# Performance work log

Hardware: AMD Instinct MI355X
Metric: run time of the kernel (lower is better)

The kernel has to match this reference:

```python
import jax, jax.numpy as jnp
import numpy as np

B, N, D, H, DK = 4, 2048, 1024, 16, 64  # batch, seq, model_dim, heads, key_dim (= value_dim)
NEG = -1e9


def setup_inputs() -> dict:
    key = jax.random.key(0)
    ks = jax.random.split(key, 5)
    X = jax.random.normal(ks[0], (B, N, D), dtype=jnp.float32)
    # causal additive mask [N, N]; module slices mask[:N, :M] and adds to logits
    mask = jnp.where(jnp.tril(jnp.ones((N, N), dtype=bool)), 0.0, NEG).astype(jnp.float32)
    s = 1.0 / np.sqrt(D)
    Wq = jax.random.normal(ks[1], (D, H * DK), dtype=jnp.float32) * s
    Wk = jax.random.normal(ks[2], (D, H * DK), dtype=jnp.float32) * s
    Wv = jax.random.normal(ks[3], (D, H * DK), dtype=jnp.float32) * s
    Wo = jax.random.normal(ks[4], (H * DK, D), dtype=jnp.float32) * s
    return {"X": X, "mask": mask, "Wq": Wq, "Wk": Wk, "Wv": Wv, "Wo": Wo}


def reference(X, mask, Wq, Wk, Wv, Wo):
    # Linear projections (bias=False), then split heads: [B,N,H,DK] -> [B,H,N,DK]
    Q = (X @ Wq).reshape(B, N, H, DK).transpose(0, 2, 1, 3)
    K = (X @ Wk).reshape(B, N, H, DK).transpose(0, 2, 1, 3)
    V = (X @ Wv).reshape(B, N, H, DK).transpose(0, 2, 1, 3)
    # full [B,H,N,N] attention logits (module materializes it explicitly)
    att = jnp.einsum('bhnd,bhmd->bhnm', Q, K) / jnp.sqrt(jnp.float32(DK))
    # dropout is in eval mode here -> identity; then additive mask[:N,:M]
    att = att + mask[:N, :N]
    prob = jax.nn.softmax(att, axis=-1)
    values = jnp.einsum('bhnm,bhmd->bhnd', prob, V)
    values_cat = values.transpose(0, 2, 1, 3).reshape(B, N, H * DK)
    return values_cat @ Wo
```

## Files before the change

### kernel.cpp

```cpp
#include <hip/hip_runtime.h>

typedef __fp16   f2  __attribute__((ext_vector_type(2)));
typedef _Float16 h4  __attribute__((ext_vector_type(4)));
typedef _Float16 v8h __attribute__((ext_vector_type(8)));
typedef float    v4f __attribute__((ext_vector_type(4)));
struct f2x2 { f2 lo, hi; };

#if __has_builtin(__builtin_amdgcn_exp2f)
#define FEXP2(x) __builtin_amdgcn_exp2f(x)
#else
#define FEXP2(x) exp2f(x)
#endif

constexpr int Bn = 4, Nn = 2048, Dn = 1024, Hn = 16, DKn = 64, Mn = 8192;

__device__ __forceinline__ void load_lds16(const _Float16* g, _Float16* l) {
    __builtin_amdgcn_global_load_lds(
        (const __attribute__((address_space(1))) void*)g,
        (__attribute__((address_space(3))) void*)l, 16, 0, 0);
}

__global__ __launch_bounds__(256) void cast_f16(const float* __restrict__ x,
                                                _Float16* __restrict__ y) {
    const int i = blockIdx.x * 256 + threadIdx.x;
    const float4 v = ((const float4*)x)[i];
    h4 o; o[0] = (_Float16)v.x; o[1] = (_Float16)v.y;
    o[2] = (_Float16)v.z; o[3] = (_Float16)v.w;
    ((h4*)y)[i] = o;
}

__global__ __launch_bounds__(256) void castW4(const float* __restrict__ Wq,
                                              const float* __restrict__ Wk,
                                              const float* __restrict__ Wv,
                                              const float* __restrict__ Wo,
                                              _Float16* __restrict__ Wqkv,
                                              _Float16* __restrict__ Wto) {
    __shared__ float tile[32][33];
    const int which = blockIdx.x >> 10, bid = blockIdx.x & 1023;
    const float* W = which == 0 ? Wq : which == 1 ? Wk : which == 2 ? Wv : Wo;
    _Float16* Dst = which < 3 ? (Wqkv + ((size_t)which << 20)) : Wto;
    const int bx = bid & 31, by = bid >> 5;
    const int t = threadIdx.x;
    const int r = t >> 3, c4 = (t & 7) * 4;
    const float4 v = *(const float4*)&W[(size_t)(by * 32 + r) * Dn + bx * 32 + c4];
    tile[r][c4 + 0] = v.x; tile[r][c4 + 1] = v.y;
    tile[r][c4 + 2] = v.z; tile[r][c4 + 3] = v.w;
    __syncthreads();
    h4 o;
    o[0] = (_Float16)tile[c4 + 0][r];
    o[1] = (_Float16)tile[c4 + 1][r];
    o[2] = (_Float16)tile[c4 + 2][r];
    o[3] = (_Float16)tile[c4 + 3][r];
    *(h4*)&Dst[(size_t)(bx * 32 + r) * Dn + by * 32 + c4] = o;
}

#define MFMA16(A, B, C) __builtin_amdgcn_mfma_f32_16x16x32_f16((A), (B), (C), 0, 0, 0)

#define GEMM_PIPE_SETUP(MF_, NF_, BN_, WME, WNE, VMS)                            \
    constexpr int MF = MF_, NF = NF_, BNc = BN_;                                 \
    constexpr int BREG = BNc * 32;                     \
    __shared__ __align__(16) _Float16 As[4 * 8192];                              \
    __shared__ __align__(16) _Float16 Bs[4 * BREG];                              \
    const int t = threadIdx.x, lane = t & 63, w = t >> 6;                        \
    const int quad = lane >> 4, l16 = lane & 15;                                 \
    const int wm = (WME), wn = (WNE);                                            \
                        \
    const int rA = t >> 2;                                                       \
    const int gc = ((t & 3) ^ ((t >> 3) & 3)) * 8;  \
    const _Float16* pA0 = Abase + (size_t)rA * Dn + gc;                          \
    const _Float16* pA1 = pA0 + (size_t)128 * Dn;           \
    const _Float16* pB0 = Bbase + (size_t)rA * Dn + gc;                          \
    const _Float16* pB1 = pB0 + (size_t)128 * Dn;   \
    auto stage = [&](int ts, int sh) {                                           \
        const int reg = (ts & 1) * 2 + sh;                                       \
        const int ko  = ts * 64 + sh * 32;                                       \
        load_lds16(pA0 + ko, As + reg * 8192 + w * 512);                         \
        load_lds16(pA1 + ko, As + reg * 8192 + 4096 + w * 512);                  \
        load_lds16(pB0 + ko, Bs + reg * BREG + w * 512);                         \
        if (BNc == 256) load_lds16(pB1 + ko, Bs + reg * BREG + 4096 + w * 512);  \
    };                                                                           \
             \
    const int swz  = (quad ^ ((l16 >> 1) & 3)) * 8;                              \
    const int aoff = (wm * (MF * 16) + l16) * 32 + swz;                          \
    const int boff = (wn * (NF * 16) + l16) * 32 + swz;                          \
    v4f acc[MF][NF];                                                             \
    _Pragma("unroll") for (int i = 0; i < MF; ++i)                               \
        _Pragma("unroll") for (int j = 0; j < NF; ++j) acc[i][j] = v4f{0, 0, 0, 0};\
    stage(0, 0); stage(0, 1); stage(1, 0);            \
    asm volatile("s_waitcnt " VMS ::: "memory");                                 \
    __builtin_amdgcn_s_barrier();

#define GPHASE(BUF, KH, TS, SH, DOST, VM) do {                                   \
    const _Float16* Ab_ = As + ((BUF) * 2 + (KH)) * 8192 + aoff;                 \
    const _Float16* Bb_ = Bs + ((BUF) * 2 + (KH)) * BREG + boff;                 \
    v8h a_[MF], b_[NF];                                                          \
    _Pragma("unroll") for (int i = 0; i < MF; ++i)                               \
        a_[i] = *(const v8h*)(Ab_ + i * 512);                                    \
    _Pragma("unroll") for (int j = 0; j < NF; ++j)                               \
        b_[j] = *(const v8h*)(Bb_ + j * 512);                                    \
    if (DOST) stage((TS), (SH));                                                 \
    __builtin_amdgcn_s_barrier();                                                \
    __builtin_amdgcn_s_setprio(1);                                               \
    _Pragma("unroll") for (int i = 0; i < MF; ++i)                               \
        _Pragma("unroll") for (int j = 0; j < NF; ++j)                           \
            acc[i][j] = MFMA16(a_[i], b_[j], acc[i][j]);                         \
    __builtin_amdgcn_s_setprio(0);                                               \
    asm volatile("s_waitcnt " VM ::: "memory");                                  \
    __builtin_amdgcn_s_barrier();                                                \
} while (0)

#define GEMM_PIPE_KLOOP(VMS, VMT)                                                \
    for (int tt = 0; tt < 14; tt += 2) {                                         \
        GPHASE(0, 0, tt + 1, 1, true, VMS);                                      \
        GPHASE(0, 1, tt + 2, 0, true, VMS);                                      \
        GPHASE(1, 0, tt + 2, 1, true, VMS);                                      \
        GPHASE(1, 1, tt + 3, 0, true, VMS);                                      \
    }                                                                            \
    GPHASE(0, 0, 15, 1, true,  VMS);              \
    GPHASE(0, 1, 0, 0, false, VMT);                                    \
    GPHASE(1, 0, 0, 0, false, "vmcnt(0)");                             \
    GPHASE(1, 1, 0, 0, false, "vmcnt(0)");

__global__ __launch_bounds__(512) void gemmqkv(const _Float16* __restrict__ A,
                                               const _Float16* __restrict__ Wt,
                                               _Float16* __restrict__ Qo,
                                               _Float16* __restrict__ Ko,
                                               _Float16* __restrict__ Vo)
{
    const int bx = blockIdx.x % 12, by = blockIdx.x / 12;
    const int m0 = by * 256, n0 = bx * 256;
    const _Float16* Abase = A + (size_t)m0 * Dn;
    const _Float16* Bbase = Wt + (size_t)n0 * Dn;

    GEMM_PIPE_SETUP(8, 4, 256, w >> 2, w & 3, "vmcnt(8)")
    GEMM_PIPE_KLOOP("vmcnt(8)", "vmcnt(4)")

    const int sec = n0 >> 10;
    if (sec < 2) {
        _Float16* C = sec ? Ko : Qo;
        const float scale = sec ? 1.0f : 0.125f * 1.44269504f;
#pragma unroll
        for (int mf = 0; mf < MF; ++mf) {
            const int mbase = m0 + wm * 128 + mf * 16 + quad * 4;
#pragma unroll
            for (int nf = 0; nf < NF; ++nf) {
                const int nl = (n0 + wn * 64 + nf * 16 + l16) & 1023;
                const int h = nl >> 6, dk = nl & 63;
#pragma unroll
                for (int r = 0; r < 4; ++r) {
                    const int m = mbase + r, b = m >> 11, nr = m & (Nn - 1);
                    C[((size_t)(b * Hn + h) * Nn + nr) * DKn + dk] = (_Float16)(acc[mf][nf][r] * scale);
                }
            }
        }
    } else {
#pragma unroll
        for (int mf = 0; mf < MF; ++mf) {
            const int mbase = m0 + wm * 128 + mf * 16 + quad * 4;
            const int b = mbase >> 11, nr = mbase & (Nn - 1);
#pragma unroll
            for (int nf = 0; nf < NF; ++nf) {
                const int nl = (n0 + wn * 64 + nf * 16 + l16) & 1023;
                const int h = nl >> 6, dk = nl & 63;
                h4 o; o[0] = (_Float16)acc[mf][nf][0]; o[1] = (_Float16)acc[mf][nf][1];
                o[2] = (_Float16)acc[mf][nf][2]; o[3] = (_Float16)acc[mf][nf][3];
                *(h4*)&Vo[((size_t)(b * Hn + h) * DKn + dk) * Nn + nr] = o;
            }
        }
    }
}

__global__ __launch_bounds__(512) void gemmo(const _Float16* __restrict__ A,
                                             const _Float16* __restrict__ Wt,
                                             float* __restrict__ C)
{
    const int bx = blockIdx.x & 7, by = blockIdx.x >> 3;
    const int m0 = by * 256, n0 = bx * 128;
    const _Float16* Abase = A + (size_t)m0 * Dn;
    const _Float16* Bbase = Wt + (size_t)n0 * Dn;

    GEMM_PIPE_SETUP(4, 4, 128, w & 3, w >> 2, "vmcnt(6)")
    GEMM_PIPE_KLOOP("vmcnt(6)", "vmcnt(3)")

#pragma unroll
    for (int mf = 0; mf < MF; ++mf) {
        const int mbase = m0 + wm * 64 + mf * 16 + quad * 4;
#pragma unroll
        for (int nf = 0; nf < NF; ++nf) {
            const int n = n0 + wn * 64 + nf * 16 + l16;
#pragma unroll
            for (int r = 0; r < 4; ++r)
                C[(size_t)(mbase + r) * Dn + n] = acc[mf][nf][r];
        }
    }
}

__global__ __launch_bounds__(256) void flashv5(const _Float16* __restrict__ Q,
                                               const _Float16* __restrict__ K,
                                               const _Float16* __restrict__ Vt,
                                               _Float16* __restrict__ O)
{
    __shared__ __align__(16) _Float16 KS[64 * 64];
    __shared__ __align__(16) _Float16 VS[64 * 64];
    __shared__ __align__(16) _Float16 Ps[4][32 * 64];

    const int t = threadIdx.x;
    const int lane = t & 63, w = t >> 6;
    const int quad = lane >> 4, l16 = lane & 15;
    const int bh = blockIdx.x & 63;
    const int qtile = 15 - (blockIdx.x >> 6);
    const int b = bh >> 4, h = bh & 15;
    const int qb = qtile * 128 + w * 32;

    const _Float16* Qg = Q  + (size_t)bh * Nn * DKn;
    const _Float16* Kg = K  + (size_t)bh * Nn * DKn;
    const _Float16* Vg = Vt + (size_t)bh * DKn * Nn;

    auto stage = [&](int kt) {
        const int k0 = kt * 64;
#pragma unroll
        for (int jj = 0; jj < 2; ++jj) {
            const int ci = jj * 256 + w * 64 + lane;
            const int r = ci >> 3, c = ci & 7;
            const int gc = (c ^ (r & 7)) * 8;
            load_lds16(Kg + (size_t)(k0 + r) * DKn + gc, &KS[(jj * 256 + w * 64) * 8]);
            load_lds16(Vg + (size_t)r * Nn + k0 + gc,    &VS[(jj * 256 + w * 64) * 8]);
        }
    };
#define SWZ(arr, r, c) (*(const v8h*)&(arr)[(r) * 64 + (((c) ^ ((r) & 7)) * 8)])

    v8h qf[2][2];
#pragma unroll
    for (int qq = 0; qq < 2; ++qq)
#pragma unroll
        for (int ks = 0; ks < 2; ++ks)
            qf[qq][ks] = *(const v8h*)&Qg[(size_t)(qb + qq * 16 + l16) * DKn + ks * 32 + quad * 8];

    v8h ones;
#pragma unroll
    for (int i = 0; i < 8; ++i) ones[i] = (_Float16)1.0f;

    v4f o[2][4];
#pragma unroll
    for (int mq = 0; mq < 2; ++mq)
#pragma unroll
        for (int nt = 0; nt < 4; ++nt) o[mq][nt] = v4f{0.f, 0.f, 0.f, 0.f};
    v4f ol[2] = {v4f{0.f, 0.f, 0.f, 0.f}, v4f{0.f, 0.f, 0.f, 0.f}};

    const int NKT  = 2 * qtile + 2;
    const int diag = 2 * qtile + (w >> 1);

    for (int kt = 0; kt < NKT; ++kt) {
        stage(kt);
        __syncthreads();
        if (kt <= diag) {
            const int k0 = kt * 64;
            auto ptile = [&](bool domask) {
#pragma unroll
                for (int kk = 0; kk < 4; ++kk) {
                    v4f s0 = v4f{0.f, 0.f, 0.f, 0.f}, s1 = v4f{0.f, 0.f, 0.f, 0.f};
#pragma unroll
                    for (int ks = 0; ks < 2; ++ks) {
                        const v8h ak = SWZ(KS, kk * 16 + l16, ks * 4 + quad);
                        s0 = __builtin_amdgcn_mfma_f32_16x16x32_f16(ak, qf[0][ks], s0, 0, 0, 0);
                        s1 = __builtin_amdgcn_mfma_f32_16x16x32_f16(ak, qf[1][ks], s1, 0, 0, 0);
                    }
                    const int key0 = k0 + kk * 16 + quad * 4;
#pragma unroll
                    for (int qq = 0; qq < 2; ++qq) {
                        const v4f sv = qq ? s1 : s0;
                        const int q = qb + qq * 16 + l16;
                        float p[4];
#pragma unroll
                        for (int r = 0; r < 4; ++r) {
                            float x = sv[r];
                            if (domask) x = (key0 + r > q) ? -1e9f : x;
                            p[r] = FEXP2(x);
                        }
                        f2x2 pkr;
                        pkr.lo = __builtin_amdgcn_cvt_pkrtz(p[0], p[1]);
                        pkr.hi = __builtin_amdgcn_cvt_pkrtz(p[2], p[3]);
                        const h4 pk = __builtin_bit_cast(h4, pkr);
                        const int prow = qq * 16 + l16;
                        const int pch  = kk * 2 + (quad >> 1);
                        *(h4*)&Ps[w][prow * 64 + ((pch ^ (prow & 7)) * 8 + (quad & 1) * 4)] = pk;
                    }
                }
#pragma unroll
                for (int ks = 0; ks < 2; ++ks)
#pragma unroll
                    for (int mq = 0; mq < 2; ++mq) {
                        const int arow = mq * 16 + l16;
                        const int ach  = ks * 4 + quad;
                        const v8h a = *(const v8h*)&Ps[w][arow * 64 + ((ach ^ (arow & 7)) * 8)];
#pragma unroll
                        for (int nt = 0; nt < 4; ++nt) {
                            const v8h bvv = SWZ(VS, nt * 16 + l16, ks * 4 + quad);
                            o[mq][nt] = __builtin_amdgcn_mfma_f32_16x16x32_f16(a, bvv, o[mq][nt], 0, 0, 0);
                        }
                        ol[mq] = __builtin_amdgcn_mfma_f32_16x16x32_f16(a, ones, ol[mq], 0, 0, 0);
                    }
            };
            if (kt == diag) ptile(true); else ptile(false);
        }
        __syncthreads();
    }
#undef SWZ

    _Float16* Op = O + (size_t)b * Nn * Dn + h * DKn;
#pragma unroll
    for (int mq = 0; mq < 2; ++mq)
#pragma unroll
        for (int r = 0; r < 4; ++r) {
            const float li = 1.0f / ol[mq][r];
            const int qrow = qb + mq * 16 + quad * 4 + r;
#pragma unroll
            for (int nt = 0; nt < 4; ++nt)
                Op[(size_t)qrow * Dn + nt * 16 + l16] = (_Float16)(o[mq][nt][r] * li);
        }
}

extern "C" void kernel_launch(void* const* d_in, const int* in_sizes, int n_in,
                              void* d_out, int out_size, void* d_ws, size_t ws_size,
                              hipStream_t stream)
{
    const float* X  = (const float*)d_in[0];
    const float* Wq = (const float*)d_in[2];
    const float* Wk = (const float*)d_in[3];
    const float* Wv = (const float*)d_in[4];
    const float* Wo = (const float*)d_in[5];

    char* ws = (char*)d_ws;
    _Float16* Xh   = (_Float16*)ws;
    _Float16* Wqkv = (_Float16*)(ws + (16u << 20));
    _Float16* Wto  = Wqkv + (3u << 20);
    _Float16* Qh   = Wto + (1u << 20);
    _Float16* Kh   = Qh + (size_t)Mn * Dn;
    _Float16* Vth  = Kh + (size_t)Mn * Dn;
    _Float16* Ah   = Vth + (size_t)Mn * Dn;

    cast_f16<<<(Mn * Dn / 4) / 256, 256, 0, stream>>>(X, Xh);
    castW4<<<4096, 256, 0, stream>>>(Wq, Wk, Wv, Wo, Wqkv, Wto);
    gemmqkv<<<384, 512, 0, stream>>>(Xh, Wqkv, Qh, Kh, Vth);
    flashv5<<<1024, 256, 0, stream>>>(Qh, Kh, Vth, Ah);
    gemmo<<<256, 512, 0, stream>>>(Ah, Wto, (float*)d_out);
}
```

Before: 262.1 us.

## Double-buffer GEMM LDS fragment reads in registers to overlap with MFMA

The GEMM k-loop now loads the next LDS fragment set into a second register bank while the MFMAs run on the previous set, and drops the mid-phase barrier between the LDS read and the compute. The vmcnt waits are tightened because each phase now reads one region ahead, so global loads must land earlier. This aims to hide LDS read latency behind matrix math, at the cost of more VGPRs for the doubled fragment registers and less slack for global-load latency.

```diff
diff --git a/kernel.cpp b/kernel.cpp
--- a/kernel.cpp
+++ b/kernel.cpp
@@ -86,40 +86,47 @@
     v4f acc[MF][NF];                                                             \
     _Pragma("unroll") for (int i = 0; i < MF; ++i)                               \
         _Pragma("unroll") for (int j = 0; j < NF; ++j) acc[i][j] = v4f{0, 0, 0, 0};\
+    v8h aR0[MF], aR1[MF], bR0[NF], bR1[NF];                                      \
     stage(0, 0); stage(0, 1); stage(1, 0);            \
-    asm volatile("s_waitcnt " VMS ::: "memory");                                 \
-    __builtin_amdgcn_s_barrier();
-
-#define GPHASE(BUF, KH, TS, SH, DOST, VM) do {                                   \
-    const _Float16* Ab_ = As + ((BUF) * 2 + (KH)) * 8192 + aoff;                 \
-    const _Float16* Bb_ = Bs + ((BUF) * 2 + (KH)) * BREG + boff;                 \
-    v8h a_[MF], b_[NF];                                                          \
+    asm volatile("s_waitcnt " VMS ::: "memory");         \
+    __builtin_amdgcn_s_barrier();                                                \
+    GRD(0, 0);
+
+#define GRD(SET, REG) do {                                                       \
+    const _Float16* Ab_ = As + (REG) * 8192 + aoff;                              \
+    const _Float16* Bb_ = Bs + (REG) * BREG + boff;                              \
     _Pragma("unroll") for (int i = 0; i < MF; ++i)                               \
-        a_[i] = *(const v8h*)(Ab_ + i * 512);                                    \
+        aR##SET[i] = *(const v8h*)(Ab_ + i * 512);                               \
     _Pragma("unroll") for (int j = 0; j < NF; ++j)                               \
-        b_[j] = *(const v8h*)(Bb_ + j * 512);                                    \
-    if (DOST) stage((TS), (SH));                                                 \
-    __builtin_amdgcn_s_barrier();                                                \
+        bR##SET[j] = *(const v8h*)(Bb_ + j * 512);                               \
+} while (0)
+
+#define GMM(SET)                                                                 \
     __builtin_amdgcn_s_setprio(1);                                               \
     _Pragma("unroll") for (int i = 0; i < MF; ++i)                               \
         _Pragma("unroll") for (int j = 0; j < NF; ++j)                           \
-            acc[i][j] = MFMA16(a_[i], b_[j], acc[i][j]);                         \
-    __builtin_amdgcn_s_setprio(0);                                               \
+            acc[i][j] = MFMA16(aR##SET[i], bR##SET[j], acc[i][j]);               \
+    __builtin_amdgcn_s_setprio(0);
+
+#define GPHASE(RSET, RREG, MSET, TS, SH, DOST, VM) do {                          \
+    GRD(RSET, RREG);                                                             \
+    if (DOST) stage((TS), (SH));                                                 \
+    GMM(MSET)                                                                    \
     asm volatile("s_waitcnt " VM ::: "memory");                                  \
     __builtin_amdgcn_s_barrier();                                                \
 } while (0)
 
-#define GEMM_PIPE_KLOOP(VMS, VMT)                                                \
+#define GEMM_PIPE_KLOOP(VMS)                                                     \
     for (int tt = 0; tt < 14; tt += 2) {                                         \
-        GPHASE(0, 0, tt + 1, 1, true, VMS);                                      \
-        GPHASE(0, 1, tt + 2, 0, true, VMS);                                      \
-        GPHASE(1, 0, tt + 2, 1, true, VMS);                                      \
-        GPHASE(1, 1, tt + 3, 0, true, VMS);                                      \
+        GPHASE(1, 1, 0, tt + 1, 1, true, VMS);                                   \
+        GPHASE(0, 2, 1, tt + 2, 0, true, VMS);                                   \
+        GPHASE(1, 3, 0, tt + 2, 1, true, VMS);                                   \
+        GPHASE(0, 0, 1, tt + 3, 0, true, VMS);                                   \
     }                                                                            \
-    GPHASE(0, 0, 15, 1, true,  VMS);              \
-    GPHASE(0, 1, 0, 0, false, VMT);                                    \
-    GPHASE(1, 0, 0, 0, false, "vmcnt(0)");                             \
-    GPHASE(1, 1, 0, 0, false, "vmcnt(0)");
+    GPHASE(1, 1, 0, 15, 1, true,  VMS);           \
+    GPHASE(0, 2, 1, 0, 0, false, "vmcnt(0)");                          \
+    GPHASE(1, 3, 0, 0, 0, false, "vmcnt(0)");                          \
+    GMM(1)
 
 __global__ __launch_bounds__(512) void gemmqkv(const _Float16* __restrict__ A,
                                                const _Float16* __restrict__ Wt,
@@ -132,8 +139,8 @@
     const _Float16* Abase = A + (size_t)m0 * Dn;
     const _Float16* Bbase = Wt + (size_t)n0 * Dn;
 
-    GEMM_PIPE_SETUP(8, 4, 256, w >> 2, w & 3, "vmcnt(8)")
-    GEMM_PIPE_KLOOP("vmcnt(8)", "vmcnt(4)")
+    GEMM_PIPE_SETUP(8, 4, 256, w >> 2, w & 3, "vmcnt(4)")
+    GEMM_PIPE_KLOOP("vmcnt(4)")
 
     const int sec = n0 >> 10;
     if (sec < 2) {
@@ -179,8 +186,8 @@
     const _Float16* Abase = A + (size_t)m0 * Dn;
     const _Float16* Bbase = Wt + (size_t)n0 * Dn;
 
-    GEMM_PIPE_SETUP(4, 4, 128, w & 3, w >> 2, "vmcnt(6)")
-    GEMM_PIPE_KLOOP("vmcnt(6)", "vmcnt(3)")
+    GEMM_PIPE_SETUP(4, 4, 128, w & 3, w >> 2, "vmcnt(3)")
+    GEMM_PIPE_KLOOP("vmcnt(3)")
 
 #pragma unroll
     for (int mf = 0; mf < MF; ++mf) {
```

Result: slower. 275.5 us (+5.1%).

## Split QKV GEMM k-step into two half-phases to cut register pressure

Applied to the files above, without the earlier changes.

Replaces the shared GEMM macros with per-kernel code. The QKV GEMM now loads the A fragments in two halves of four, with a barrier between the MFMA groups, and splits the global-to-LDS staging of A and B across the two halves. Both GEMMs get launch_bounds(512, 2) and explicit lgkmcnt waits. The goal is fewer live VGPRs so two blocks can share a CU, and better interleaving of loads with MFMA work. The cost is extra barriers per k-step and tighter register budgets that may cause spills.

```diff
diff --git a/kernel.cpp b/kernel.cpp
--- a/kernel.cpp
+++ b/kernel.cpp
@@ -56,94 +56,104 @@
 
 #define MFMA16(A, B, C) __builtin_amdgcn_mfma_f32_16x16x32_f16((A), (B), (C), 0, 0, 0)
 
-#define GEMM_PIPE_SETUP(MF_, NF_, BN_, WME, WNE, VMS)                            \
-    constexpr int MF = MF_, NF = NF_, BNc = BN_;                                 \
-    constexpr int BREG = BNc * 32;                     \
-    __shared__ __align__(16) _Float16 As[4 * 8192];                              \
-    __shared__ __align__(16) _Float16 Bs[4 * BREG];                              \
-    const int t = threadIdx.x, lane = t & 63, w = t >> 6;                        \
-    const int quad = lane >> 4, l16 = lane & 15;                                 \
-    const int wm = (WME), wn = (WNE);                                            \
-                        \
-    const int rA = t >> 2;                                                       \
-    const int gc = ((t & 3) ^ ((t >> 3) & 3)) * 8;  \
-    const _Float16* pA0 = Abase + (size_t)rA * Dn + gc;                          \
-    const _Float16* pA1 = pA0 + (size_t)128 * Dn;           \
-    const _Float16* pB0 = Bbase + (size_t)rA * Dn + gc;                          \
-    const _Float16* pB1 = pB0 + (size_t)128 * Dn;   \
-    auto stage = [&](int ts, int sh) {                                           \
-        const int reg = (ts & 1) * 2 + sh;                                       \
-        const int ko  = ts * 64 + sh * 32;                                       \
-        load_lds16(pA0 + ko, As + reg * 8192 + w * 512);                         \
-        load_lds16(pA1 + ko, As + reg * 8192 + 4096 + w * 512);                  \
-        load_lds16(pB0 + ko, Bs + reg * BREG + w * 512);                         \
-        if (BNc == 256) load_lds16(pB1 + ko, Bs + reg * BREG + 4096 + w * 512);  \
-    };                                                                           \
-             \
-    const int swz  = (quad ^ ((l16 >> 1) & 3)) * 8;                              \
-    const int aoff = (wm * (MF * 16) + l16) * 32 + swz;                          \
-    const int boff = (wn * (NF * 16) + l16) * 32 + swz;                          \
-    v4f acc[MF][NF];                                                             \
-    _Pragma("unroll") for (int i = 0; i < MF; ++i)                               \
-        _Pragma("unroll") for (int j = 0; j < NF; ++j) acc[i][j] = v4f{0, 0, 0, 0};\
-    stage(0, 0); stage(0, 1); stage(1, 0);            \
-    asm volatile("s_waitcnt " VMS ::: "memory");                                 \
-    __builtin_amdgcn_s_barrier();
-
-#define GPHASE(BUF, KH, TS, SH, DOST, VM) do {                                   \
-    const _Float16* Ab_ = As + ((BUF) * 2 + (KH)) * 8192 + aoff;                 \
-    const _Float16* Bb_ = Bs + ((BUF) * 2 + (KH)) * BREG + boff;                 \
-    v8h a_[MF], b_[NF];                                                          \
-    _Pragma("unroll") for (int i = 0; i < MF; ++i)                               \
-        a_[i] = *(const v8h*)(Ab_ + i * 512);                                    \
-    _Pragma("unroll") for (int j = 0; j < NF; ++j)                               \
-        b_[j] = *(const v8h*)(Bb_ + j * 512);                                    \
-    if (DOST) stage((TS), (SH));                                                 \
-    __builtin_amdgcn_s_barrier();                                                \
-    __builtin_amdgcn_s_setprio(1);                                               \
-    _Pragma("unroll") for (int i = 0; i < MF; ++i)                               \
-        _Pragma("unroll") for (int j = 0; j < NF; ++j)                           \
-            acc[i][j] = MFMA16(a_[i], b_[j], acc[i][j]);                         \
-    __builtin_amdgcn_s_setprio(0);                                               \
-    asm volatile("s_waitcnt " VM ::: "memory");                                  \
-    __builtin_amdgcn_s_barrier();                                                \
-} while (0)
-
-#define GEMM_PIPE_KLOOP(VMS, VMT)                                                \
-    for (int tt = 0; tt < 14; tt += 2) {                                         \
-        GPHASE(0, 0, tt + 1, 1, true, VMS);                                      \
-        GPHASE(0, 1, tt + 2, 0, true, VMS);                                      \
-        GPHASE(1, 0, tt + 2, 1, true, VMS);                                      \
-        GPHASE(1, 1, tt + 3, 0, true, VMS);                                      \
-    }                                                                            \
-    GPHASE(0, 0, 15, 1, true,  VMS);              \
-    GPHASE(0, 1, 0, 0, false, VMT);                                    \
-    GPHASE(1, 0, 0, 0, false, "vmcnt(0)");                             \
-    GPHASE(1, 1, 0, 0, false, "vmcnt(0)");
-
-__global__ __launch_bounds__(512) void gemmqkv(const _Float16* __restrict__ A,
-                                               const _Float16* __restrict__ Wt,
-                                               _Float16* __restrict__ Qo,
-                                               _Float16* __restrict__ Ko,
-                                               _Float16* __restrict__ Vo)
+__global__ __launch_bounds__(512, 2) void gemmqkv(const _Float16* __restrict__ A,
+                                                  const _Float16* __restrict__ Wt,
+                                                  _Float16* __restrict__ Qo,
+                                                  _Float16* __restrict__ Ko,
+                                                  _Float16* __restrict__ Vo)
 {
+    __shared__ __align__(16) _Float16 As[4 * 8192];
+    __shared__ __align__(16) _Float16 Bs[4 * 8192];
     const int bx = blockIdx.x % 12, by = blockIdx.x / 12;
     const int m0 = by * 256, n0 = bx * 256;
     const _Float16* Abase = A + (size_t)m0 * Dn;
     const _Float16* Bbase = Wt + (size_t)n0 * Dn;
 
-    GEMM_PIPE_SETUP(8, 4, 256, w >> 2, w & 3, "vmcnt(8)")
-    GEMM_PIPE_KLOOP("vmcnt(8)", "vmcnt(4)")
+    const int t = threadIdx.x, lane = t & 63, w = t >> 6;
+    const int quad = lane >> 4, l16 = lane & 15;
+    const int wm = w >> 2, wn = w & 3;
+    const int rA = t >> 2;
+    const int gc = ((t & 3) ^ ((t >> 3) & 3)) * 8;
+    const _Float16* pA0 = Abase + (size_t)rA * Dn + gc;
+    const _Float16* pA1 = pA0 + (size_t)128 * Dn;
+    const _Float16* pB0 = Bbase + (size_t)rA * Dn + gc;
+    const _Float16* pB1 = pB0 + (size_t)128 * Dn;
+    auto stageA = [&](int ts, int sh) {
+        const int reg = (ts & 1) * 2 + sh, ko = ts * 64 + sh * 32;
+        load_lds16(pA0 + ko, As + reg * 8192 + w * 512);
+        load_lds16(pA1 + ko, As + reg * 8192 + 4096 + w * 512);
+    };
+    auto stageB = [&](int ts, int sh) {
+        const int reg = (ts & 1) * 2 + sh, ko = ts * 64 + sh * 32;
+        load_lds16(pB0 + ko, Bs + reg * 8192 + w * 512);
+        load_lds16(pB1 + ko, Bs + reg * 8192 + 4096 + w * 512);
+    };
+    const int swz  = (quad ^ ((l16 >> 1) & 3)) * 8;
+    const int aoff = (wm * 128 + l16) * 32 + swz;
+    const int boff = (wn * 64 + l16) * 32 + swz;
+
+    v4f acc[8][4];
+#pragma unroll
+    for (int i = 0; i < 8; ++i)
+#pragma unroll
+        for (int j = 0; j < 4; ++j) acc[i][j] = v4f{0.f, 0.f, 0.f, 0.f};
+
+    stageA(0, 0); stageB(0, 0); stageA(0, 1); stageB(0, 1); stageA(1, 0); stageB(1, 0);
+    asm volatile("s_waitcnt vmcnt(8)" ::: "memory");
+    __builtin_amdgcn_s_barrier();
+
+#define QKV_KSTEP(REG, TS, SH, DOST, VM, DOVM) do {                              \
+    const _Float16* Ab_ = As + (REG) * 8192 + aoff;                              \
+    const _Float16* Bb_ = Bs + (REG) * 8192 + boff;                              \
+    v8h aL[4], aH[4], bL[4];                                                     \
+    _Pragma("unroll") for (int q2 = 0; q2 < 4; ++q2) {                           \
+        aL[q2] = *(const v8h*)(Ab_ + q2 * 512);                                  \
+        bL[q2] = *(const v8h*)(Bb_ + q2 * 512);                                  \
+    }                                                                            \
+    if (DOST) stageA((TS), (SH));                                                \
+    __builtin_amdgcn_s_barrier();                                                \
+    asm volatile("s_waitcnt lgkmcnt(0)" ::: "memory");                           \
+    __builtin_amdgcn_s_setprio(1);                                               \
+    _Pragma("unroll") for (int i2 = 0; i2 < 4; ++i2)                             \
+        _Pragma("unroll") for (int j2 = 0; j2 < 4; ++j2)                         \
+            acc[i2][j2] = MFMA16(aL[i2], bL[j2], acc[i2][j2]);                   \
+    __builtin_amdgcn_s_setprio(0);                                               \
+    __builtin_amdgcn_s_barrier();                                                \
+    _Pragma("unroll") for (int q2 = 0; q2 < 4; ++q2)                             \
+        aH[q2] = *(const v8h*)(Ab_ + 2048 + q2 * 512);                           \
+    if (DOST) stageB((TS), (SH));                                                \
+    __builtin_amdgcn_s_barrier();                                                \
+    asm volatile("s_waitcnt lgkmcnt(0)" ::: "memory");                           \
+    __builtin_amdgcn_s_setprio(1);                                               \
+    _Pragma("unroll") for (int i2 = 0; i2 < 4; ++i2)                             \
+        _Pragma("unroll") for (int j2 = 0; j2 < 4; ++j2)                         \
+            acc[4 + i2][j2] = MFMA16(aH[i2], bL[j2], acc[4 + i2][j2]);           \
+    __builtin_amdgcn_s_setprio(0);                                               \
+    if (DOVM) asm volatile("s_waitcnt " VM ::: "memory");                        \
+    __builtin_amdgcn_s_barrier();                                                \
+} while (0)
+
+    for (int tt = 0; tt < 14; tt += 2) {
+        QKV_KSTEP(0, tt + 1, 1, true, "vmcnt(8)", true);
+        QKV_KSTEP(1, tt + 2, 0, true, "vmcnt(8)", true);
+        QKV_KSTEP(2, tt + 2, 1, true, "vmcnt(8)", true);
+        QKV_KSTEP(3, tt + 3, 0, true, "vmcnt(8)", true);
+    }
+    QKV_KSTEP(0, 15, 1, true,  "vmcnt(8)", true);
+    QKV_KSTEP(1, 0, 0, false, "vmcnt(4)", true);
+    QKV_KSTEP(2, 0, 0, false, "vmcnt(0)", true);
+    QKV_KSTEP(3, 0, 0, false, "vmcnt(0)", false);
+#undef QKV_KSTEP
 
     const int sec = n0 >> 10;
     if (sec < 2) {
         _Float16* C = sec ? Ko : Qo;
         const float scale = sec ? 1.0f : 0.125f * 1.44269504f;
 #pragma unroll
-        for (int mf = 0; mf < MF; ++mf) {
+        for (int mf = 0; mf < 8; ++mf) {
             const int mbase = m0 + wm * 128 + mf * 16 + quad * 4;
 #pragma unroll
-            for (int nf = 0; nf < NF; ++nf) {
+            for (int nf = 0; nf < 4; ++nf) {
                 const int nl = (n0 + wn * 64 + nf * 16 + l16) & 1023;
                 const int h = nl >> 6, dk = nl & 63;
 #pragma unroll
@@ -155,11 +165,11 @@
         }
     } else {
 #pragma unroll
-        for (int mf = 0; mf < MF; ++mf) {
+        for (int mf = 0; mf < 8; ++mf) {
             const int mbase = m0 + wm * 128 + mf * 16 + quad * 4;
             const int b = mbase >> 11, nr = mbase & (Nn - 1);
 #pragma unroll
-            for (int nf = 0; nf < NF; ++nf) {
+            for (int nf = 0; nf < 4; ++nf) {
                 const int nl = (n0 + wn * 64 + nf * 16 + l16) & 1023;
                 const int h = nl >> 6, dk = nl & 63;
                 h4 o; o[0] = (_Float16)acc[mf][nf][0]; o[1] = (_Float16)acc[mf][nf][1];
@@ -170,23 +180,82 @@
     }
 }
 
-__global__ __launch_bounds__(512) void gemmo(const _Float16* __restrict__ A,
-                                             const _Float16* __restrict__ Wt,
-                                             float* __restrict__ C)
+__global__ __launch_bounds__(512, 2) void gemmo(const _Float16* __restrict__ A,
+                                                const _Float16* __restrict__ Wt,
+                                                float* __restrict__ C)
 {
+    __shared__ __align__(16) _Float16 As[4 * 8192];
+    __shared__ __align__(16) _Float16 Bs[4 * 4096];
     const int bx = blockIdx.x & 7, by = blockIdx.x >> 3;
     const int m0 = by * 256, n0 = bx * 128;
     const _Float16* Abase = A + (size_t)m0 * Dn;
     const _Float16* Bbase = Wt + (size_t)n0 * Dn;
 
-    GEMM_PIPE_SETUP(4, 4, 128, w & 3, w >> 2, "vmcnt(6)")
-    GEMM_PIPE_KLOOP("vmcnt(6)", "vmcnt(3)")
-
-#pragma unroll
-    for (int mf = 0; mf < MF; ++mf) {
+    const int t = threadIdx.x, lane = t & 63, w = t >> 6;
+    const int quad = lane >> 4, l16 = lane & 15;
+    const int wm = w & 3, wn = w >> 2;
+    const int rA = t >> 2;
+    const int gc = ((t & 3) ^ ((t >> 3) & 3)) * 8;
+    const _Float16* pA0 = Abase + (size_t)rA * Dn + gc;
+    const _Float16* pA1 = pA0 + (size_t)128 * Dn;
+    const _Float16* pB0 = Bbase + (size_t)rA * Dn + gc;
+    auto stage3 = [&](int ts, int sh) {
+        const int reg = (ts & 1) * 2 + sh, ko = ts * 64 + sh * 32;
+        load_lds16(pA0 + ko, As + reg * 8192 + w * 512);
+        load_lds16(pA1 + ko, As + reg * 8192 + 4096 + w * 512);
+        load_lds16(pB0 + ko, Bs + reg * 4096 + w * 512);
+    };
+    const int swz  = (quad ^ ((l16 >> 1) & 3)) * 8;
+    const int aoff = (wm * 64 + l16) * 32 + swz;
+    const int boff = (wn * 64 + l16) * 32 + swz;
+
+    v4f acc[4][4];
+#pragma unroll
+    for (int i = 0; i < 4; ++i)
+#pragma unroll
+        for (int j = 0; j < 4; ++j) acc[i][j] = v4f{0.f, 0.f, 0.f, 0.f};
+
+    stage3(0, 0); stage3(0, 1); stage3(1, 0);
+    asm volatile("s_waitcnt vmcnt(6)" ::: "memory");
+    __builtin_amdgcn_s_barrier();
+
+#define O_KSTEP(REG, TS, SH, DOST, VM, DOVM) do {                                \
+    const _Float16* Ab_ = As + (REG) * 8192 + aoff;                              \
+    const _Float16* Bb_ = Bs + (REG) * 4096 + boff;                              \
+    v8h aL[4], bL[4];                                                            \
+    _Pragma("unroll") for (int q2 = 0; q2 < 4; ++q2) {                           \
+        aL[q2] = *(const v8h*)(Ab_ + q2 * 512);                                  \
+        bL[q2] = *(const v8h*)(Bb_ + q2 * 512);                                  \
+    }                                                                            \
+    if (DOST) stage3((TS), (SH));                                                \
+    __builtin_amdgcn_s_barrier();                                                \
+    asm volatile("s_waitcnt lgkmcnt(0)" ::: "memory");                           \
+    __builtin_amdgcn_s_setprio(1);                                               \
+    _Pragma("unroll") for (int i2 = 0; i2 < 4; ++i2)                             \
+        _Pragma("unroll") for (int j2 = 0; j2 < 4; ++j2)                         \
+            acc[i2][j2] = MFMA16(aL[i2], bL[j2], acc[i2][j2]);                   \
+    __builtin_amdgcn_s_setprio(0);                                               \
+    if (DOVM) asm volatile("s_waitcnt " VM ::: "memory");                        \
+    __builtin_amdgcn_s_barrier();                                                \
+} while (0)
+
+    for (int tt = 0; tt < 14; tt += 2) {
+        O_KSTEP(0, tt + 1, 1, true, "vmcnt(6)", true);
+        O_KSTEP(1, tt + 2, 0, true, "vmcnt(6)", true);
+        O_KSTEP(2, tt + 2, 1, true, "vmcnt(6)", true);
+        O_KSTEP(3, tt + 3, 0, true, "vmcnt(6)", true);
+    }
+    O_KSTEP(0, 15, 1, true,  "vmcnt(6)", true);
+    O_KSTEP(1, 0, 0, false, "vmcnt(3)", true);
+    O_KSTEP(2, 0, 0, false, "vmcnt(0)", true);
+    O_KSTEP(3, 0, 0, false, "vmcnt(0)", false);
+#undef O_KSTEP
+
+#pragma unroll
+    for (int mf = 0; mf < 4; ++mf) {
         const int mbase = m0 + wm * 64 + mf * 16 + quad * 4;
 #pragma unroll
-        for (int nf = 0; nf < NF; ++nf) {
+        for (int nf = 0; nf < 4; ++nf) {
             const int n = n0 + wn * 64 + nf * 16 + l16;
 #pragma unroll
             for (int r = 0; r < 4; ++r)
```

Result: no change. 261.3 us (-0.3%).
